# Kernel optimization log

Hardware: AMD Instinct MI355X
Metric: run time of the kernel (lower is better)

The kernel has to match this reference:

```python
import jax, jax.numpy as jnp
import numpy as np

B, L, H = 16, 2048, 768
INNER = max(H // 2, 32)
RADIUS = 2
K_STEPS = 4
ETA = 0.1
ETA_DECAY = 0.9
MU_MAX = 10.0
LAM = 0.1


def _window_edges(length, radius):
    ei, ej = [], []
    for r in range(1, radius + 1):
        i = np.arange(length - r)
        ei.append(i)
        ej.append(i + r)
    return (jnp.asarray(np.concatenate(ei), jnp.int32),
            jnp.asarray(np.concatenate(ej), jnp.int32))


def setup_inputs() -> dict:
    key = jax.random.key(0)
    ks = jax.random.split(key, 6)
    hidden = jax.random.normal(ks[0], (B, L, H), jnp.float32)
    attention_mask = jnp.ones((B, L), jnp.int32)  # uniform full lengths -> single bucket, window path
    w1 = jax.random.normal(ks[1], (2, INNER), jnp.float32) * 0.2
    b1 = jnp.zeros((INNER,), jnp.float32)
    w2 = jax.random.normal(ks[2], (INNER, 1), jnp.float32) * 0.05
    b2 = jnp.zeros((1,), jnp.float32)
    wq = jax.random.normal(ks[3], (H, H), jnp.float32) * (1.0 / np.sqrt(H))
    bq = jnp.zeros((H,), jnp.float32)
    gamma = jnp.ones((H,), jnp.float32)
    beta = jnp.zeros((H,), jnp.float32)
    edges_i, edges_j = _window_edges(L, RADIUS)
    return dict(hidden=hidden, attention_mask=attention_mask, w1=w1, b1=b1,
                w2=w2, b2=b2, wq=wq, bq=bq, gamma=gamma, beta=beta,
                edges_i=edges_i, edges_j=edges_j)


def _friction(hidden, w1, b1, w2, b2, wq, bq, gamma, beta, edges_i, edges_j):
    eps = 1e-6
    q = hidden @ wq + bq                      # [B,L,H]
    state = hidden
    mu = None
    for step in range(K_STEPS):
        # edge weights from current state (recompute_mu=True)
        h_i = state[:, edges_i]               # [B,E,H] gather
        h_j = state[:, edges_j]
        diff = h_i - h_j
        dist = jnp.sqrt(jnp.sum(diff * diff, -1))
        n_i = jnp.maximum(jnp.sqrt(jnp.sum(h_i * h_i, -1)), eps)
        n_j = jnp.maximum(jnp.sqrt(jnp.sum(h_j * h_j, -1)), eps)
        cos = jnp.sum(h_i * h_j, -1) / (n_i * n_j)
        feats = jnp.stack([dist, cos], -1)    # [B,E,2]
        mid = jax.nn.gelu(feats @ w1 + b1, approximate=False)
        mu = jnp.minimum(jax.nn.softplus((mid @ w2 + b2)[..., 0]) + 1e-5, MU_MAX)  # [B,E]
        # normalized weighted graph Laplacian applied to state
        w = mu[..., None] * diff
        deg = jnp.zeros((state.shape[0], state.shape[1]), state.dtype)
        deg = deg.at[:, edges_i].add(mu).at[:, edges_j].add(mu)
        inv = jnp.maximum(deg, 1e-6) ** -0.5
        w = w * (inv[:, edges_i] * inv[:, edges_j])[..., None]
        lap = jnp.zeros_like(state).at[:, edges_i].add(w).at[:, edges_j].add(-w)
        state = state - (ETA * ETA_DECAY ** step) * (lap - q)
        # 1D chain smoothing with replicated boundaries
        left = jnp.concatenate([state[:, :1], state[:, :-1]], 1)
        right = jnp.concatenate([state[:, 1:], state[:, -1:]], 1)
        state = state - LAM * (2 * state - left - right)
    # edge energy with last mu and final state: 0.5 * sum_e mu_e ||s_i - s_j||^2
    df = state[:, edges_i] - state[:, edges_j]
    energy = 0.5 * jnp.sum(mu * jnp.sum(df * df, -1), axis=1)  # [B]
    res = state + hidden
    mean = jnp.mean(res, -1, keepdims=True)
    var = jnp.mean((res - mean) ** 2, -1, keepdims=True)
    out = (res - mean) / jnp.sqrt(var + 1e-5) * gamma + beta
    return out, energy


def reference(hidden, attention_mask, w1, b1, w2, b2, wq, bq, gamma, beta, edges_i, edges_j):
    # all masks are full-length ones -> single bucket, batched window path
    return _friction(hidden, w1, b1, w2, b2, wq, bq, gamma, beta, edges_i, edges_j)
```

## Files before the change

kernel.cpp:

```cpp
#include <hip/hip_runtime.h>
#include <hip/hip_bf16.h>
#include <math.h>

#define B_ 16
#define L_ 2048
#define H_ 768
#define INNER_ 384
#define MU_MAX_ 10.0f
#define LAM_ 0.1f
#define EDGES_ (2 * L_ - 3)

typedef short v8bf __attribute__((ext_vector_type(8)));
typedef float v4f  __attribute__((ext_vector_type(4)));

static __device__ __forceinline__ float wave_sum(float v) {
    #pragma unroll
    for (int o = 32; o > 0; o >>= 1) v += __shfl_xor(v, o, 64);
    return v;
}

static __device__ __forceinline__ float dot4(const float4& a, const float4& b) {
    return a.x * b.x + a.y * b.y + a.z * b.z + a.w * b.w;
}

static __device__ __forceinline__ void fma4(float4& a, float c, float4 x) {
    a.x = fmaf(c, x.x, a.x); a.y = fmaf(c, x.y, a.y);
    a.z = fmaf(c, x.z, a.z); a.w = fmaf(c, x.w, a.w);
}

static __device__ __forceinline__ ushort f2bf(float x) {
    unsigned u = __float_as_uint(x);
    u += 0x7fffu + ((u >> 16) & 1u);
    return (ushort)(u >> 16);
}

__global__ __launch_bounds__(256) void conv_wqt_kernel(
    const float* __restrict__ wq, ushort* __restrict__ wt)
{
    __shared__ float tile[64][65];
    int k0 = blockIdx.x * 64, n0 = blockIdx.y * 64;
    int t = threadIdx.x;
    #pragma unroll
    for (int it = 0; it < 16; ++it) {
        int lin = t + it * 256;
        int r = lin >> 6, c = lin & 63;
        tile[r][c] = wq[(size_t)(k0 + r) * H_ + n0 + c];
    }
    __syncthreads();
    #pragma unroll
    for (int it = 0; it < 16; ++it) {
        int lin = t + it * 256;
        int r = lin >> 6, c = lin & 63;
        wt[(size_t)(n0 + r) * H_ + k0 + c] = f2bf(tile[c][r]);
    }
}

#define GBM 128
#define GBN 128
#define GBK 64
#define LSTR 72

__global__ __launch_bounds__(256) void gemm_q_kernel(
    const float* __restrict__ A32, const ushort* __restrict__ Wt,
    const float* __restrict__ bias, float* __restrict__ C)
{
    __shared__ ushort As[GBM * LSTR];
    __shared__ ushort Bs[GBN * LSTR];
    const int K = H_, N = H_;
    int m0 = blockIdx.y * GBM;
    int n0 = blockIdx.x * GBN;
    int t = threadIdx.x;
    int lane = t & 63, w = t >> 6;
    int wm = (w & 1) * 64, wn = (w >> 1) * 64;
    int row16 = lane & 15, quad = lane >> 4;

    v4f acc[4][4];
    #pragma unroll
    for (int i = 0; i < 4; ++i)
        #pragma unroll
        for (int j = 0; j < 4; ++j)
            acc[i][j] = (v4f){0.f, 0.f, 0.f, 0.f};

    for (int k0 = 0; k0 < K; k0 += GBK) {
        #pragma unroll
        for (int it = 0; it < 4; ++it) {
            int lin = t + it * 256;
            int r = lin >> 3;
            int s = lin & 7;
            const float* ap = A32 + (size_t)(m0 + r) * K + k0 + s * 8;
            float4 f0 = *(const float4*)ap;
            float4 f1 = *(const float4*)(ap + 4);
            ushort tmp[8] = { f2bf(f0.x), f2bf(f0.y), f2bf(f0.z), f2bf(f0.w),
                              f2bf(f1.x), f2bf(f1.y), f2bf(f1.z), f2bf(f1.w) };
            *(v8bf*)&As[r * LSTR + s * 8] = *(v8bf*)tmp;
            *(v8bf*)&Bs[r * LSTR + s * 8] =
                *(const v8bf*)(Wt + (size_t)(n0 + r) * K + k0 + s * 8);
        }
        __syncthreads();
        #pragma unroll
        for (int h = 0; h < 2; ++h) {
            v8bf af[4], bf[4];
            #pragma unroll
            for (int i = 0; i < 4; ++i)
                af[i] = *(v8bf*)&As[(wm + i * 16 + row16) * LSTR + h * 32 + quad * 8];
            #pragma unroll
            for (int j = 0; j < 4; ++j)
                bf[j] = *(v8bf*)&Bs[(wn + j * 16 + row16) * LSTR + h * 32 + quad * 8];
            #pragma unroll
            for (int i = 0; i < 4; ++i)
                #pragma unroll
                for (int j = 0; j < 4; ++j)
                    acc[i][j] = __builtin_amdgcn_mfma_f32_16x16x32_bf16(
                        af[i], bf[j], acc[i][j], 0, 0, 0);
        }
        __syncthreads();
    }
    #pragma unroll
    for (int j = 0; j < 4; ++j) {
        int ncol = n0 + wn + j * 16 + row16;
        float bqv = bias[ncol];
        #pragma unroll
        for (int i = 0; i < 4; ++i) {
            int mrow = m0 + wm + i * 16 + quad * 4;
            #pragma unroll
            for (int r = 0; r < 4; ++r)
                C[(size_t)(mrow + r) * N + ncol] = acc[i][j][r] + bqv;
        }
    }
}

static __device__ __forceinline__ float mu_mlp2(
    float si, float sj, float dotij,
    const float* w1d, const float* w1c, const float* b1v, const float* w2v,
    float b2v)
{
    float dist = sqrtf(fmaxf(si + sj - 2.f * dotij, 0.f));
    float cosv = dotij / (fmaxf(sqrtf(si), 1e-6f) * fmaxf(sqrtf(sj), 1e-6f));
    float acc = 0.f;
    #pragma unroll
    for (int k = 0; k < 6; ++k) {
        float z = fmaf(dist, w1d[k], fmaf(cosv, w1c[k], b1v[k]));
        float g = 0.5f * z * (1.f + erff(z * 0.70710678118654752f));
        acc = fmaf(g, w2v[k], acc);
    }
    acc = wave_sum(acc) + b2v;
    float sp = fmaxf(acc, 0.f) + log1pf(expf(-fabsf(acc)));
    return fminf(sp + 1e-5f, MU_MAX_);
}

__global__ __launch_bounds__(256) void mu_pair_kernel(
    const float* __restrict__ src,
    const float* __restrict__ w1, const float* __restrict__ b1,
    const float* __restrict__ w2, const float* __restrict__ b2,
    float* __restrict__ mu)
{
    int blk = blockIdx.x;
    int chunk = (blk & 7) * ((B_ * L_ / 8) / 8) + (blk >> 3);
    int b = chunk >> 8;
    int p0 = (chunk & 255) * 8;
    int w = threadIdx.x >> 6, lane = threadIdx.x & 63;
    int t0 = p0 + 2 * w;

    const float* sB = src + (size_t)b * L_ * H_;
    int r2 = min(t0 + 2, L_ - 1), r3 = min(t0 + 3, L_ - 1);
    const float4* x0p = (const float4*)(sB + (size_t)t0 * H_);
    const float4* x1p = (const float4*)(sB + (size_t)(t0 + 1) * H_);
    const float4* x2p = (const float4*)(sB + (size_t)r2 * H_);
    const float4* x3p = (const float4*)(sB + (size_t)r3 * H_);

    float ss0 = 0.f, ss1 = 0.f, ss2 = 0.f, ss3 = 0.f;
    float d1a = 0.f, d1b = 0.f, d2a = 0.f, d2b = 0.f;
    #pragma unroll
    for (int ch = 0; ch < 3; ++ch) {
        int off = ch * 64 + lane;
        float4 x0 = x0p[off], x1 = x1p[off], x2 = x2p[off], x3 = x3p[off];
        ss0 += dot4(x0, x0); ss1 += dot4(x1, x1);
        ss2 += dot4(x2, x2); ss3 += dot4(x3, x3);
        d1a += dot4(x0, x1); d1b += dot4(x1, x2);
        d2a += dot4(x0, x2); d2b += dot4(x1, x3);
    }
    ss0 = wave_sum(ss0); ss1 = wave_sum(ss1); ss2 = wave_sum(ss2);
    d1a = wave_sum(d1a); d1b = wave_sum(d1b); d2a = wave_sum(d2a);

    float w1d[6], w1c[6], b1v[6], w2v[6];
    #pragma unroll
    for (int k = 0; k < 6; ++k) {
        int u = k * 64 + lane;
        w1d[k] = w1[u]; w1c[k] = w1[INNER_ + u]; b1v[k] = b1[u]; w2v[k] = w2[u];
    }
    float b2v = b2[0];
    float* mB = mu + (size_t)b * EDGES_;

    float m1a = mu_mlp2(ss0, ss1, d1a, w1d, w1c, b1v, w2v, b2v);
    if (lane == 0) mB[t0] = m1a;
    if (t0 < L_ - 2) {
        float m2a_ = mu_mlp2(ss0, ss2, d2a, w1d, w1c, b1v, w2v, b2v);
        if (lane == 0) mB[(L_ - 1) + t0] = m2a_;
        float m1b = mu_mlp2(ss1, ss2, d1b, w1d, w1c, b1v, w2v, b2v);
        if (lane == 0) mB[t0 + 1] = m1b;
        if (t0 + 1 < L_ - 2) {
            ss3 = wave_sum(ss3); d2b = wave_sum(d2b);
            float m2b = mu_mlp2(ss1, ss3, d2b, w1d, w1c, b1v, w2v, b2v);
            if (lane == 0) mB[(L_ - 1) + t0 + 1] = m2b;
        }
    }
}

static __device__ __forceinline__ void row_coeffs(
    int p, const float* __restrict__ mp, float coef, float C[7], float e[3])
{
    float m1a[8];
    #pragma unroll
    for (int j = 0; j < 8; ++j) {
        int u = p - 4 + j;
        m1a[j] = (u >= 0 && u < L_ - 1) ? mp[u] : 0.f;
    }
    float m2a[9];
    #pragma unroll
    for (int j = 0; j < 9; ++j) {
        int u = p - 5 + j;
        m2a[j] = (u >= 0 && u < L_ - 2) ? mp[(L_ - 1) + u] : 0.f;
    }
    float invv[7];
    #pragma unroll
    for (int d = 0; d < 7; ++d) {
        int u = p - 3 + d;
        if (u < 0 || u >= L_) { invv[d] = 0.f; }
        else {
            float deg = m1a[d + 1] + m1a[d] + m2a[d + 2] + m2a[d];
            invv[d] = 1.f / sqrtf(fmaxf(deg, 1e-6f));
        }
    }
    float gwv[3];
    gwv[0] = (p == 0) ? 0.f : LAM_;
    gwv[2] = (p == L_ - 1) ? 0.f : LAM_;
    gwv[1] = 1.f - 2.f * LAM_ + ((p == 0 || p == L_ - 1) ? LAM_ : 0.f);
    #pragma unroll
    for (int d = 0; d < 7; ++d) C[d] = 0.f;
    #pragma unroll
    for (int i = 0; i < 3; ++i) {
        float g = gwv[i];
        float wm2 = m2a[i + 2] * invv[i + 2] * invv[i];
        float wm1 = m1a[i + 2] * invv[i + 2] * invv[i + 1];
        float wp1 = m1a[i + 3] * invv[i + 2] * invv[i + 3];
        float wp2 = m2a[i + 4] * invv[i + 2] * invv[i + 4];
        float wsum = wm2 + wm1 + wp1 + wp2;
        C[i]     = fmaf(g * coef, wm2, C[i]);
        C[i + 1] = fmaf(g * coef, wm1, C[i + 1]);
        C[i + 2] = fmaf(g, fmaf(-coef, wsum, 1.f), C[i + 2]);
        C[i + 3] = fmaf(g * coef, wp1, C[i + 3]);
        C[i + 4] = fmaf(g * coef, wp2, C[i + 4]);
        e[i] = g * coef;
    }
}

static __device__ __forceinline__ void ln_store(
    const float4 rr[3], const float* __restrict__ hrow,
    const float* __restrict__ gamma, const float* __restrict__ beta,
    float* __restrict__ orow, int lane)
{
    float sum = 0.f, sq = 0.f;
    float4 v[3];
    #pragma unroll
    for (int ch = 0; ch < 3; ++ch) {
        int off = ch * 64 + lane;
        float4 h = ((const float4*)hrow)[off];
        float4 x = rr[ch];
        x.x += h.x; x.y += h.y; x.z += h.z; x.w += h.w;
        v[ch] = x;
        sum += x.x + x.y + x.z + x.w;
        sq  += x.x * x.x + x.y * x.y + x.z * x.z + x.w * x.w;
    }
    sum = wave_sum(sum); sq = wave_sum(sq);
    float mean = sum * (1.f / H_);
    float var  = sq * (1.f / H_) - mean * mean;
    float rs = 1.f / sqrtf(var + 1e-5f);
    #pragma unroll
    for (int ch = 0; ch < 3; ++ch) {
        int off = ch * 64 + lane;
        float4 g4 = ((const float4*)gamma)[off];
        float4 b4 = ((const float4*)beta)[off];
        float4 o;
        o.x = (v[ch].x - mean) * rs * g4.x + b4.x;
        o.y = (v[ch].y - mean) * rs * g4.y + b4.y;
        o.z = (v[ch].z - mean) * rs * g4.z + b4.z;
        o.w = (v[ch].w - mean) * rs * g4.w + b4.w;
        ((float4*)orow)[off] = o;
    }
}

template <int LN>
__global__ __launch_bounds__(256) void upd_pair_kernel(
    const float* __restrict__ src, const float* __restrict__ q,
    const float* __restrict__ mu, float* __restrict__ dst,
    const float* __restrict__ hidden, const float* __restrict__ gamma,
    const float* __restrict__ beta, float* __restrict__ lnout, float coef)
{
    int blk = blockIdx.x;
    int chunk = (blk & 7) * ((B_ * L_ / 8) / 8) + (blk >> 3);
    int b = chunk >> 8;
    int p0 = (chunk & 255) * 8;
    int w = threadIdx.x >> 6, lane = threadIdx.x & 63;
    int t0 = p0 + 2 * w;

    const float* mp = mu + (size_t)b * EDGES_;
    const float* sB = src + (size_t)b * L_ * H_;
    const float* qB = q + (size_t)b * L_ * H_;

    float CA[7], eA[3], CB[7], eB[3];
    row_coeffs(t0, mp, coef, CA, eA);
    row_coeffs(t0 + 1, mp, coef, CB, eB);

    const float* sp[8];
    #pragma unroll
    for (int u = 0; u < 8; ++u) {
        int g = min(max(t0 - 3 + u, 0), L_ - 1);
        sp[u] = sB + (size_t)g * H_;
    }
    const float* qp[4];
    #pragma unroll
    for (int u = 0; u < 4; ++u) {
        int g = min(max(t0 - 1 + u, 0), L_ - 1);
        qp[u] = qB + (size_t)g * H_;
    }

    float* dA = dst + ((size_t)b * L_ + t0) * H_;
    float4 keepA[3], keepB[3];
    #pragma unroll
    for (int ch = 0; ch < 3; ++ch) {
        int off = ch * 64 + lane;
        float4 S[8], Q[4];
        #pragma unroll
        for (int u = 0; u < 8; ++u) S[u] = ((const float4*)sp[u])[off];
        #pragma unroll
        for (int u = 0; u < 4; ++u) Q[u] = ((const float4*)qp[u])[off];
        float4 a = {0.f, 0.f, 0.f, 0.f}, c2 = {0.f, 0.f, 0.f, 0.f};
        #pragma unroll
        for (int d = 0; d < 7; ++d) { fma4(a, CA[d], S[d]); fma4(c2, CB[d], S[d + 1]); }
        #pragma unroll
        for (int i = 0; i < 3; ++i) { fma4(a, eA[i], Q[i]); fma4(c2, eB[i], Q[i + 1]); }
        ((float4*)dA)[off] = a;
        ((float4*)(dA + H_))[off] = c2;
        if (LN) { keepA[ch] = a; keepB[ch] = c2; }
    }

    if (LN) {
        size_t rowA = (size_t)b * L_ + t0;
        ln_store(keepA, hidden + rowA * H_, gamma, beta, lnout + rowA * H_, lane);
        ln_store(keepB, hidden + (rowA + 1) * H_, gamma, beta,
                 lnout + (rowA + 1) * H_, lane);
    }
}

__global__ void zero_energy_kernel(float* __restrict__ e) {
    if (threadIdx.x < B_) e[threadIdx.x] = 0.f;
}

#define EPW 16
__global__ __launch_bounds__(256) void energy_kernel(
    const float* __restrict__ state, const int* __restrict__ ei, const int* __restrict__ ej,
    const float* __restrict__ mu, float* __restrict__ energy, int E)
{
    __shared__ float red[4];
    int wib = threadIdx.x >> 6;
    int lane = threadIdx.x & 63;
    int nchunk = (E + 63) / 64;
    int b = blockIdx.x / nchunk;
    int chunk = blockIdx.x - b * nchunk;
    int e0 = chunk * 64 + wib * EPW;
    const float* base = state + (size_t)b * L_ * H_;
    const float* muB = mu + (size_t)b * E;
    float part = 0.f;
    for (int k = 0; k < EPW; ++k) {
        int e = e0 + k;
        if (e >= E) break;
        int i = ei[e], j = ej[e];
        const float4* ri = (const float4*)(base + (size_t)i * H_);
        const float4* rj = (const float4*)(base + (size_t)j * H_);
        float s = 0.f;
        #pragma unroll
        for (int it = 0; it < 3; ++it) {
            float4 xi = ri[it * 64 + lane], xj = rj[it * 64 + lane];
            float dx = xi.x - xj.x, dy = xi.y - xj.y, dz = xi.z - xj.z, dw = xi.w - xj.w;
            s += dx*dx + dy*dy + dz*dz + dw*dw;
        }
        s = wave_sum(s);
        part += muB[e] * s;
    }
    if (lane == 0) red[wib] = part;
    __syncthreads();
    if (threadIdx.x == 0)
        atomicAdd(energy + b, 0.5f * (red[0] + red[1] + red[2] + red[3]));
}

extern "C" void kernel_launch(void* const* d_in, const int* in_sizes, int n_in,
                              void* d_out, int out_size, void* d_ws, size_t ws_size,
                              hipStream_t stream)
{
    const float* hidden = (const float*)d_in[0];
    const float* w1 = (const float*)d_in[2];
    const float* b1 = (const float*)d_in[3];
    const float* w2 = (const float*)d_in[4];
    const float* b2 = (const float*)d_in[5];
    const float* wq = (const float*)d_in[6];
    const float* bq = (const float*)d_in[7];
    const float* gamma = (const float*)d_in[8];
    const float* beta  = (const float*)d_in[9];
    const int* ei = (const int*)d_in[10];
    const int* ej = (const int*)d_in[11];
    int E = in_sizes[10];

    const size_t BLH = (size_t)B_ * L_ * H_;
    float* out = (float*)d_out;
    float* energy = out + BLH;

    float* q    = (float*)d_ws;
    float* bufA = q + BLH;
    float* bufB = bufA + BLH;
    float* mu   = bufB + BLH;
    ushort* wt  = (ushort*)(mu + (size_t)B_ * EDGES_);

    conv_wqt_kernel<<<dim3(H_ / 64, H_ / 64), 256, 0, stream>>>(wq, wt);
    gemm_q_kernel<<<dim3(H_ / GBN, (B_ * L_) / GBM), 256, 0, stream>>>(hidden, wt, bq, q);
    zero_energy_kernel<<<1, 64, 0, stream>>>(energy);

    const int NBP = B_ * L_ / 8;
    float coef = 0.1f;

    mu_pair_kernel<<<NBP, 256, 0, stream>>>(hidden, w1, b1, w2, b2, mu);
    upd_pair_kernel<0><<<NBP, 256, 0, stream>>>(hidden, q, mu, bufA,
        hidden, gamma, beta, nullptr, coef);
    coef *= 0.9f;
    mu_pair_kernel<<<NBP, 256, 0, stream>>>(bufA, w1, b1, w2, b2, mu);
    upd_pair_kernel<0><<<NBP, 256, 0, stream>>>(bufA, q, mu, bufB,
        hidden, gamma, beta, nullptr, coef);
    coef *= 0.9f;
    mu_pair_kernel<<<NBP, 256, 0, stream>>>(bufB, w1, b1, w2, b2, mu);
    upd_pair_kernel<0><<<NBP, 256, 0, stream>>>(bufB, q, mu, bufA,
        hidden, gamma, beta, nullptr, coef);
    coef *= 0.9f;
    mu_pair_kernel<<<NBP, 256, 0, stream>>>(bufA, w1, b1, w2, b2, mu);
    upd_pair_kernel<1><<<NBP, 256, 0, stream>>>(bufA, q, mu, bufB,
        hidden, gamma, beta, out, coef);

    int nchunk = (E + 63) / 64;
    energy_kernel<<<B_ * nchunk, 256, 0, stream>>>(bufB, ei, ej, mu, energy, E);
}
```

Baseline: 800.7 us.

## Batch mu MLP over four rows per wave and prefetch A tiles in Q GEMM

The mu kernel now has each wave handle four rows, loading six rows to compute eight edge features at once. Each GELU weight load is then amortized over eight edges, and the final softplus is done by lane 0 only, which cuts redundant row loads and per-edge weight fetches. The Q GEMM adds a register prefetch of the next A tile, drops the B shared-memory tile in favor of direct global loads of bf16 weights, and remaps block indices for L2 locality. Reading weights straight from global may add latency, and the wider mu kernel raises register pressure.

```diff
diff --git a/kernel.cpp b/kernel.cpp
--- a/kernel.cpp
+++ b/kernel.cpp
@@ -65,10 +65,11 @@
     const float* __restrict__ bias, float* __restrict__ C)
 {
     __shared__ ushort As[GBM * LSTR];
-    __shared__ ushort Bs[GBN * LSTR];
     const int K = H_, N = H_;
-    int m0 = blockIdx.y * GBM;
-    int n0 = blockIdx.x * GBN;
+    int idx = blockIdx.x;
+    int c = idx & 7, rest = idx >> 3;
+    int n0 = (rest % 6) * GBN;
+    int m0 = ((rest / 6) * 8 + c) * GBM;
     int t = threadIdx.x;
     int lane = t & 63, w = t >> 6;
     int wm = (w & 1) * 64, wn = (w >> 1) * 64;
@@ -81,20 +82,37 @@
         for (int j = 0; j < 4; ++j)
             acc[i][j] = (v4f){0.f, 0.f, 0.f, 0.f};
 
-    for (int k0 = 0; k0 < K; k0 += GBK) {
+    int r = t >> 1;
+    int sseg = (t & 1) * 4;
+    float4 pf0[4], pf1[4];
+    #pragma unroll
+    for (int it = 0; it < 4; ++it) {
+        int lin = t + it * 256;
+        int rr = lin >> 3, s = lin & 7;
+        const float* ap = A32 + (size_t)(m0 + rr) * K + s * 8;
+        pf0[it] = *(const float4*)ap;
+        pf1[it] = *(const float4*)(ap + 4);
+    }
+
+    for (int kt = 0; kt < 12; ++kt) {
+        int k0 = kt * GBK;
         #pragma unroll
         for (int it = 0; it < 4; ++it) {
             int lin = t + it * 256;
-            int r = lin >> 3;
-            int s = lin & 7;
-            const float* ap = A32 + (size_t)(m0 + r) * K + k0 + s * 8;
-            float4 f0 = *(const float4*)ap;
-            float4 f1 = *(const float4*)(ap + 4);
-            ushort tmp[8] = { f2bf(f0.x), f2bf(f0.y), f2bf(f0.z), f2bf(f0.w),
-                              f2bf(f1.x), f2bf(f1.y), f2bf(f1.z), f2bf(f1.w) };
-            *(v8bf*)&As[r * LSTR + s * 8] = *(v8bf*)tmp;
-            *(v8bf*)&Bs[r * LSTR + s * 8] =
-                *(const v8bf*)(Wt + (size_t)(n0 + r) * K + k0 + s * 8);
+            int rr = lin >> 3, s = lin & 7;
+            ushort tmp[8] = { f2bf(pf0[it].x), f2bf(pf0[it].y), f2bf(pf0[it].z), f2bf(pf0[it].w),
+                              f2bf(pf1[it].x), f2bf(pf1[it].y), f2bf(pf1[it].z), f2bf(pf1[it].w) };
+            *(v8bf*)&As[rr * LSTR + s * 8] = *(v8bf*)tmp;
+        }
+        if (kt < 11) {
+            #pragma unroll
+            for (int it = 0; it < 4; ++it) {
+                int lin = t + it * 256;
+                int rr = lin >> 3, s = lin & 7;
+                const float* ap = A32 + (size_t)(m0 + rr) * K + (k0 + GBK) + s * 8;
+                pf0[it] = *(const float4*)ap;
+                pf1[it] = *(const float4*)(ap + 4);
+            }
         }
         __syncthreads();
         #pragma unroll
@@ -105,7 +123,8 @@
                 af[i] = *(v8bf*)&As[(wm + i * 16 + row16) * LSTR + h * 32 + quad * 8];
             #pragma unroll
             for (int j = 0; j < 4; ++j)
-                bf[j] = *(v8bf*)&Bs[(wn + j * 16 + row16) * LSTR + h * 32 + quad * 8];
+                bf[j] = *(const v8bf*)(Wt + (size_t)(n0 + wn + j * 16 + row16) * K
+                                       + k0 + h * 32 + quad * 8);
             #pragma unroll
             for (int i = 0; i < 4; ++i)
                 #pragma unroll
@@ -123,85 +142,92 @@
         for (int i = 0; i < 4; ++i) {
             int mrow = m0 + wm + i * 16 + quad * 4;
             #pragma unroll
-            for (int r = 0; r < 4; ++r)
-                C[(size_t)(mrow + r) * N + ncol] = acc[i][j][r] + bqv;
-        }
-    }
-}
-
-static __device__ __forceinline__ float mu_mlp2(
-    float si, float sj, float dotij,
-    const float* w1d, const float* w1c, const float* b1v, const float* w2v,
-    float b2v)
-{
-    float dist = sqrtf(fmaxf(si + sj - 2.f * dotij, 0.f));
-    float cosv = dotij / (fmaxf(sqrtf(si), 1e-6f) * fmaxf(sqrtf(sj), 1e-6f));
-    float acc = 0.f;
-    #pragma unroll
-    for (int k = 0; k < 6; ++k) {
-        float z = fmaf(dist, w1d[k], fmaf(cosv, w1c[k], b1v[k]));
-        float g = 0.5f * z * (1.f + erff(z * 0.70710678118654752f));
-        acc = fmaf(g, w2v[k], acc);
-    }
-    acc = wave_sum(acc) + b2v;
-    float sp = fmaxf(acc, 0.f) + log1pf(expf(-fabsf(acc)));
-    return fminf(sp + 1e-5f, MU_MAX_);
-}
-
-__global__ __launch_bounds__(256) void mu_pair_kernel(
+            for (int rr = 0; rr < 4; ++rr)
+                C[(size_t)(mrow + rr) * N + ncol] = acc[i][j][rr] + bqv;
+        }
+    }
+}
+
+__global__ __launch_bounds__(256) void mu_quad_kernel(
     const float* __restrict__ src,
     const float* __restrict__ w1, const float* __restrict__ b1,
     const float* __restrict__ w2, const float* __restrict__ b2,
     float* __restrict__ mu)
 {
     int blk = blockIdx.x;
-    int chunk = (blk & 7) * ((B_ * L_ / 8) / 8) + (blk >> 3);
-    int b = chunk >> 8;
-    int p0 = (chunk & 255) * 8;
+    int chunk = (blk & 7) * ((B_ * L_ / 16) / 8) + (blk >> 3);
+    int b = chunk >> 7;
+    int p0 = (chunk & 127) * 16;
     int w = threadIdx.x >> 6, lane = threadIdx.x & 63;
-    int t0 = p0 + 2 * w;
+    int t0 = p0 + 4 * w;
 
     const float* sB = src + (size_t)b * L_ * H_;
-    int r2 = min(t0 + 2, L_ - 1), r3 = min(t0 + 3, L_ - 1);
-    const float4* x0p = (const float4*)(sB + (size_t)t0 * H_);
-    const float4* x1p = (const float4*)(sB + (size_t)(t0 + 1) * H_);
-    const float4* x2p = (const float4*)(sB + (size_t)r2 * H_);
-    const float4* x3p = (const float4*)(sB + (size_t)r3 * H_);
-
-    float ss0 = 0.f, ss1 = 0.f, ss2 = 0.f, ss3 = 0.f;
-    float d1a = 0.f, d1b = 0.f, d2a = 0.f, d2b = 0.f;
+    const float4* rp[6];
+    #pragma unroll
+    for (int j = 0; j < 6; ++j)
+        rp[j] = (const float4*)(sB + (size_t)min(t0 + j, L_ - 1) * H_);
+
+    float ss[6] = {0.f, 0.f, 0.f, 0.f, 0.f, 0.f};
+    float d1[4] = {0.f, 0.f, 0.f, 0.f};
+    float d2[4] = {0.f, 0.f, 0.f, 0.f};
     #pragma unroll
     for (int ch = 0; ch < 3; ++ch) {
         int off = ch * 64 + lane;
-        float4 x0 = x0p[off], x1 = x1p[off], x2 = x2p[off], x3 = x3p[off];
-        ss0 += dot4(x0, x0); ss1 += dot4(x1, x1);
-        ss2 += dot4(x2, x2); ss3 += dot4(x3, x3);
-        d1a += dot4(x0, x1); d1b += dot4(x1, x2);
-        d2a += dot4(x0, x2); d2b += dot4(x1, x3);
-    }
-    ss0 = wave_sum(ss0); ss1 = wave_sum(ss1); ss2 = wave_sum(ss2);
-    d1a = wave_sum(d1a); d1b = wave_sum(d1b); d2a = wave_sum(d2a);
-
-    float w1d[6], w1c[6], b1v[6], w2v[6];
+        float4 x[6];
+        #pragma unroll
+        for (int j = 0; j < 6; ++j) x[j] = rp[j][off];
+        #pragma unroll
+        for (int j = 0; j < 6; ++j) ss[j] += dot4(x[j], x[j]);
+        #pragma unroll
+        for (int j = 0; j < 4; ++j) {
+            d1[j] += dot4(x[j], x[j + 1]);
+            d2[j] += dot4(x[j], x[j + 2]);
+        }
+    }
+    #pragma unroll
+    for (int j = 0; j < 6; ++j) ss[j] = wave_sum(ss[j]);
+    #pragma unroll
+    for (int j = 0; j < 4; ++j) { d1[j] = wave_sum(d1[j]); d2[j] = wave_sum(d2[j]); }
+
+    float dist[8], cosv[8];
+    #pragma unroll
+    for (int e = 0; e < 4; ++e) {
+        float si = ss[e], sj = ss[e + 1], d = d1[e];
+        dist[e] = sqrtf(fmaxf(si + sj - 2.f * d, 0.f));
+        cosv[e] = d / (fmaxf(sqrtf(si), 1e-6f) * fmaxf(sqrtf(sj), 1e-6f));
+        float sk = ss[e + 2], dd = d2[e];
+        dist[4 + e] = sqrtf(fmaxf(si + sk - 2.f * dd, 0.f));
+        cosv[4 + e] = dd / (fmaxf(sqrtf(si), 1e-6f) * fmaxf(sqrtf(sk), 1e-6f));
+    }
+    float acc[8] = {0.f, 0.f, 0.f, 0.f, 0.f, 0.f, 0.f, 0.f};
     #pragma unroll
     for (int k = 0; k < 6; ++k) {
         int u = k * 64 + lane;
-        w1d[k] = w1[u]; w1c[k] = w1[INNER_ + u]; b1v[k] = b1[u]; w2v[k] = w2[u];
-    }
-    float b2v = b2[0];
-    float* mB = mu + (size_t)b * EDGES_;
-
-    float m1a = mu_mlp2(ss0, ss1, d1a, w1d, w1c, b1v, w2v, b2v);
-    if (lane == 0) mB[t0] = m1a;
-    if (t0 < L_ - 2) {
-        float m2a_ = mu_mlp2(ss0, ss2, d2a, w1d, w1c, b1v, w2v, b2v);
-        if (lane == 0) mB[(L_ - 1) + t0] = m2a_;
-        float m1b = mu_mlp2(ss1, ss2, d1b, w1d, w1c, b1v, w2v, b2v);
-        if (lane == 0) mB[t0 + 1] = m1b;
-        if (t0 + 1 < L_ - 2) {
-            ss3 = wave_sum(ss3); d2b = wave_sum(d2b);
-            float m2b = mu_mlp2(ss1, ss3, d2b, w1d, w1c, b1v, w2v, b2v);
-            if (lane == 0) mB[(L_ - 1) + t0 + 1] = m2b;
+        float wd = w1[u], wc = w1[INNER_ + u], bb = b1[u], wv = w2[u];
+        #pragma unroll
+        for (int e = 0; e < 8; ++e) {
+            float z = fmaf(dist[e], wd, fmaf(cosv[e], wc, bb));
+            float g = 0.5f * z * (1.f + erff(z * 0.70710678118654752f));
+            acc[e] = fmaf(g, wv, acc[e]);
+        }
+    }
+    #pragma unroll
+    for (int e = 0; e < 8; ++e) acc[e] = wave_sum(acc[e]);
+
+    if (lane == 0) {
+        float b2v = b2[0];
+        float* mB = mu + (size_t)b * EDGES_;
+        #pragma unroll
+        for (int e = 0; e < 4; ++e) {
+            int tt = t0 + e;
+            float a1 = acc[e] + b2v;
+            float sp1 = fmaxf(a1, 0.f) + log1pf(expf(-fabsf(a1)));
+            float m1 = fminf(sp1 + 1e-5f, MU_MAX_);
+            if (tt < L_ - 1) mB[tt] = m1;
+            float a2 = acc[4 + e] + b2v;
+            float sp2 = fmaxf(a2, 0.f) + log1pf(expf(-fabsf(a2)));
+            float m2 = fminf(sp2 + 1e-5f, MU_MAX_);
+            if (tt < L_ - 2) mB[(L_ - 1) + tt] = m2;
         }
     }
 }
@@ -421,25 +447,26 @@
     ushort* wt  = (ushort*)(mu + (size_t)B_ * EDGES_);
 
     conv_wqt_kernel<<<dim3(H_ / 64, H_ / 64), 256, 0, stream>>>(wq, wt);
-    gemm_q_kernel<<<dim3(H_ / GBN, (B_ * L_) / GBM), 256, 0, stream>>>(hidden, wt, bq, q);
+    gemm_q_kernel<<<(B_ * L_ / GBM) * (H_ / GBN), 256, 0, stream>>>(hidden, wt, bq, q);
     zero_energy_kernel<<<1, 64, 0, stream>>>(energy);
 
+    const int NBQ = B_ * L_ / 16;
     const int NBP = B_ * L_ / 8;
     float coef = 0.1f;
 
-    mu_pair_kernel<<<NBP, 256, 0, stream>>>(hidden, w1, b1, w2, b2, mu);
+    mu_quad_kernel<<<NBQ, 256, 0, stream>>>(hidden, w1, b1, w2, b2, mu);
     upd_pair_kernel<0><<<NBP, 256, 0, stream>>>(hidden, q, mu, bufA,
         hidden, gamma, beta, nullptr, coef);
     coef *= 0.9f;
-    mu_pair_kernel<<<NBP, 256, 0, stream>>>(bufA, w1, b1, w2, b2, mu);
+    mu_quad_kernel<<<NBQ, 256, 0, stream>>>(bufA, w1, b1, w2, b2, mu);
     upd_pair_kernel<0><<<NBP, 256, 0, stream>>>(bufA, q, mu, bufB,
         hidden, gamma, beta, nullptr, coef);
     coef *= 0.9f;
-    mu_pair_kernel<<<NBP, 256, 0, stream>>>(bufB, w1, b1, w2, b2, mu);
+    mu_quad_kernel<<<NBQ, 256, 0, stream>>>(bufB, w1, b1, w2, b2, mu);
     upd_pair_kernel<0><<<NBP, 256, 0, stream>>>(bufB, q, mu, bufA,
         hidden, gamma, beta, nullptr, coef);
     coef *= 0.9f;
-    mu_pair_kernel<<<NBP, 256, 0, stream>>>(bufA, w1, b1, w2, b2, mu);
+    mu_quad_kernel<<<NBQ, 256, 0, stream>>>(bufA, w1, b1, w2, b2, mu);
     upd_pair_kernel<1><<<NBP, 256, 0, stream>>>(bufA, q, mu, bufB,
         hidden, gamma, beta, out, coef);
 
```

Measured after the change: 848.9 us. 1.06x slower.

## Pre-convert activations to bf16, prefetch GEMM tiles in registers, swizzle block order

Applied to the files above, without the earlier changes.

Adds a separate pass that converts the hidden activations to bf16 into a scratch buffer, so the Q-projection GEMM reads half the bytes per tile and skips the per-tile conversion. The GEMM loop now prefetches the next K tile into registers while the current tile is computed, and uses a 1D grid with a grouped block mapping that keeps 8 M-tiles sharing each N-tile close together for L2 reuse. The extra conversion pass costs a full read and half-size write of the activations. It also raises register pressure from the prefetch buffers.

```diff
diff --git a/kernel.cpp b/kernel.cpp
--- a/kernel.cpp
+++ b/kernel.cpp
@@ -34,6 +34,18 @@
     return (ushort)(u >> 16);
 }
 
+__global__ __launch_bounds__(256) void conv_bf16_kernel(
+    const float* __restrict__ in, ushort* __restrict__ out, int n8)
+{
+    int t = blockIdx.x * 256 + threadIdx.x;
+    if (t >= n8) return;
+    float4 a = ((const float4*)in)[2 * t];
+    float4 b = ((const float4*)in)[2 * t + 1];
+    ushort r[8] = { f2bf(a.x), f2bf(a.y), f2bf(a.z), f2bf(a.w),
+                    f2bf(b.x), f2bf(b.y), f2bf(b.z), f2bf(b.w) };
+    ((v8bf*)out)[t] = *(v8bf*)r;
+}
+
 __global__ __launch_bounds__(256) void conv_wqt_kernel(
     const float* __restrict__ wq, ushort* __restrict__ wt)
 {
@@ -61,14 +73,16 @@
 #define LSTR 72
 
 __global__ __launch_bounds__(256) void gemm_q_kernel(
-    const float* __restrict__ A32, const ushort* __restrict__ Wt,
+    const ushort* __restrict__ A, const ushort* __restrict__ Wt,
     const float* __restrict__ bias, float* __restrict__ C)
 {
     __shared__ ushort As[GBM * LSTR];
     __shared__ ushort Bs[GBN * LSTR];
     const int K = H_, N = H_;
-    int m0 = blockIdx.y * GBM;
-    int n0 = blockIdx.x * GBN;
+    int idx = blockIdx.x;
+    int c = idx & 7, rest = idx >> 3;
+    int n0 = (rest % 6) * GBN;
+    int m0 = ((rest / 6) * 8 + c) * GBM;
     int t = threadIdx.x;
     int lane = t & 63, w = t >> 6;
     int wm = (w & 1) * 64, wn = (w >> 1) * 64;
@@ -81,37 +95,50 @@
         for (int j = 0; j < 4; ++j)
             acc[i][j] = (v4f){0.f, 0.f, 0.f, 0.f};
 
-    for (int k0 = 0; k0 < K; k0 += GBK) {
+    v8bf pfA[4], pfB[4];
+    #pragma unroll
+    for (int it = 0; it < 4; ++it) {
+        int lin = t + it * 256;
+        int r = lin >> 3, s = lin & 7;
+        pfA[it] = *(const v8bf*)(A  + (size_t)(m0 + r) * K + s * 8);
+        pfB[it] = *(const v8bf*)(Wt + (size_t)(n0 + r) * K + s * 8);
+    }
+
+    for (int kt = 0; kt < 12; ++kt) {
+        int k0 = kt * GBK;
         #pragma unroll
         for (int it = 0; it < 4; ++it) {
             int lin = t + it * 256;
-            int r = lin >> 3;
-            int s = lin & 7;
-            const float* ap = A32 + (size_t)(m0 + r) * K + k0 + s * 8;
-            float4 f0 = *(const float4*)ap;
-            float4 f1 = *(const float4*)(ap + 4);
-            ushort tmp[8] = { f2bf(f0.x), f2bf(f0.y), f2bf(f0.z), f2bf(f0.w),
-                              f2bf(f1.x), f2bf(f1.y), f2bf(f1.z), f2bf(f1.w) };
-            *(v8bf*)&As[r * LSTR + s * 8] = *(v8bf*)tmp;
-            *(v8bf*)&Bs[r * LSTR + s * 8] =
-                *(const v8bf*)(Wt + (size_t)(n0 + r) * K + k0 + s * 8);
+            int r = lin >> 3, s = lin & 7;
+            *(v8bf*)&As[r * LSTR + s * 8] = pfA[it];
+            *(v8bf*)&Bs[r * LSTR + s * 8] = pfB[it];
+        }
+        if (kt < 11) {
+            int kn = k0 + GBK;
+            #pragma unroll
+            for (int it = 0; it < 4; ++it) {
+                int lin = t + it * 256;
+                int r = lin >> 3, s = lin & 7;
+                pfA[it] = *(const v8bf*)(A  + (size_t)(m0 + r) * K + kn + s * 8);
+                pfB[it] = *(const v8bf*)(Wt + (size_t)(n0 + r) * K + kn + s * 8);
+            }
         }
         __syncthreads();
         #pragma unroll
         for (int h = 0; h < 2; ++h) {
-            v8bf af[4], bf[4];
+            v8bf af[4], bfv[4];
             #pragma unroll
             for (int i = 0; i < 4; ++i)
                 af[i] = *(v8bf*)&As[(wm + i * 16 + row16) * LSTR + h * 32 + quad * 8];
             #pragma unroll
             for (int j = 0; j < 4; ++j)
-                bf[j] = *(v8bf*)&Bs[(wn + j * 16 + row16) * LSTR + h * 32 + quad * 8];
+                bfv[j] = *(v8bf*)&Bs[(wn + j * 16 + row16) * LSTR + h * 32 + quad * 8];
             #pragma unroll
             for (int i = 0; i < 4; ++i)
                 #pragma unroll
                 for (int j = 0; j < 4; ++j)
                     acc[i][j] = __builtin_amdgcn_mfma_f32_16x16x32_bf16(
-                        af[i], bf[j], acc[i][j], 0, 0, 0);
+                        af[i], bfv[j], acc[i][j], 0, 0, 0);
         }
         __syncthreads();
     }
@@ -418,10 +445,13 @@
     float* bufA = q + BLH;
     float* bufB = bufA + BLH;
     float* mu   = bufB + BLH;
+    ushort* Abf = (ushort*)bufA;
     ushort* wt  = (ushort*)(mu + (size_t)B_ * EDGES_);
 
+    int n8 = (int)(BLH / 8);
+    conv_bf16_kernel<<<(n8 + 255) / 256, 256, 0, stream>>>(hidden, Abf, n8);
     conv_wqt_kernel<<<dim3(H_ / 64, H_ / 64), 256, 0, stream>>>(wq, wt);
-    gemm_q_kernel<<<dim3(H_ / GBN, (B_ * L_) / GBM), 256, 0, stream>>>(hidden, wt, bq, q);
+    gemm_q_kernel<<<(B_ * L_ / GBM) * (H_ / GBN), 256, 0, stream>>>(Abf, wt, bq, q);
     zero_energy_kernel<<<1, 64, 0, stream>>>(energy);
 
     const int NBP = B_ * L_ / 8;
```

New measurement: 777.1 us. 1.03x faster.
